# Kernel optimization log

Hardware: AMD Instinct MI355X
Metric: run time of the kernel (lower is better)

## Reference

```python
import jax, jax.numpy as jnp
import numpy as np
from jax import lax

CO, NO, ITERATIONS = 32, 8, 3
STRIDE, PADDING = 1, 1


def squash(x, axis=2):
    # x * ||x|| / (1 + ||x||^2), norm along capsule-dim axis
    norm = jnp.linalg.norm(x, axis=axis, keepdims=True)
    return x * norm / (1.0 + norm * norm)


def setup_inputs() -> dict:
    key = jax.random.key(0)
    k1, k2 = jax.random.split(key)
    x = jax.random.normal(k1, (8, 32, 8, 32, 32), dtype=jnp.float32)
    conv_w = jax.random.normal(k2, (CO * NO, 8, 3, 3), dtype=jnp.float32) * 0.05
    bias = jnp.zeros((CO, NO, 1, 1), dtype=jnp.float32)
    return {"x": x, "conv_w": conv_w, "bias": bias}


def reference(x, conv_w, bias):
    bs, ci, ni, hi, wi = x.shape
    # Conv applied per (batch, input-capsule-channel): [bs*ci, ni, hi, wi]
    xr = x.reshape(bs * ci, ni, hi, wi)
    votes = lax.conv_general_dilated(
        xr, conv_w,
        window_strides=(STRIDE, STRIDE),
        padding=[(PADDING, PADDING), (PADDING, PADDING)],
        dimension_numbers=("NCHW", "OIHW", "NCHW"))
    ho, wo = votes.shape[-2], votes.shape[-1]
    # votes: [bs, ci, co, no, ho, wo]
    votes = votes.reshape(bs, ci, CO, NO, ho, wo)
    logits = jnp.zeros((bs, ci, CO, ho, wo), dtype=votes.dtype)
    activation = None
    for _ in range(ITERATIONS):
        route = jax.nn.softmax(logits, axis=2)  # over co
        # s_j = sum_i c_ij * u_hat_{j|i} + bias -> [bs, co, no, ho, wo]
        preactivate = jnp.sum(route[:, :, :, None] * votes, axis=1) + bias
        activation = squash(preactivate, axis=2)
        # logit update: <u_hat_{j|i}, v_j> summed over no
        distances = jnp.sum(activation[:, None] * votes, axis=3)
        logits = logits + distances
    return activation
```

## Files before the change

### kernel.cpp

```cpp
#include <hip/hip_runtime.h>


typedef __attribute__((ext_vector_type(8))) short short8;
typedef __attribute__((ext_vector_type(4))) float f32x4;

#define LSTR 104
#define KP   96
#define RSTR 36

__device__ __forceinline__ ushort f2bf_rne(float f) {
    unsigned u = __float_as_uint(f);
    return (ushort)((u + 0x7fffu + ((u >> 16) & 1u)) >> 16);
}

__global__ void prep_w(const float* __restrict__ cw, ushort* __restrict__ wp) {
    int e = blockIdx.x * 256 + threadIdx.x;
    int col = e / KP, k = e - col * KP;
    float v = (k < 72) ? cw[col * 72 + k] : 0.0f;
    wp[e] = f2bf_rne(v);
}

__global__ __launch_bounds__(256, 4)
void caps_mfma2(const float* __restrict__ x,
                const ushort* __restrict__ wp,
                const float* __restrict__ bias,
                float* __restrict__ out)
{
    __shared__ ushort A[64 * LSTR];
    __shared__ float  logits[2][32 * 33];
    __shared__ float  routeT[2][32 * RSTR];

    const int t    = threadIdx.x;
    const int braw = blockIdx.x;
    const int bid = ((braw & 7) << 9) | (braw >> 3);
    const int b   = bid >> 9;
    const int q   = bid & 511;
    const int hw0 = q << 1;
    const int h   = hw0 >> 5;
    const int w0  = hw0 & 31;

    {
        const int row = t >> 2, qn = t & 3;
        const int px = row >> 5, ci = row & 31;
        const int wpx = w0 + px;
        const float* xb0 = x + (((size_t)((b * 32 + ci) * 8 + qn * 2)) << 10);
        const float* xb1 = xb0 + 1024;
        ushort hbuf[18];
        #pragma unroll
        for (int kh = 0; kh < 3; ++kh) {
            int hy = h + kh - 1;
            bool vh = (unsigned)hy < 32u;
            int base = hy << 5;
            #pragma unroll
            for (int c = 0; c < 3; ++c) {
                int wx = wpx + c - 1;
                bool ok = vh && ((unsigned)wx < 32u);
                float f0 = ok ? xb0[base + wx] : 0.0f;
                float f1 = ok ? xb1[base + wx] : 0.0f;
                hbuf[kh * 3 + c]     = f2bf_rne(f0);
                hbuf[9 + kh * 3 + c] = f2bf_rne(f1);
            }
        }
        uint* Au = reinterpret_cast<uint*>(A);
        int hbase = row * (LSTR / 2) + qn * 9;
        #pragma unroll
        for (int i = 0; i < 9; ++i)
            Au[hbase + i] = (unsigned)hbuf[2 * i] | ((unsigned)hbuf[2 * i + 1] << 16);
        int pbase = row * (LSTR / 2) + 36 + qn * 4;
        Au[pbase + 0] = 0u; Au[pbase + 1] = 0u;
        Au[pbase + 2] = 0u; Au[pbase + 3] = 0u;
    }
    __syncthreads();

    const int lane = t & 63, wv = t >> 6;
    const int lc = lane & 15, grp = lane >> 4;
    const int no = lane & 7;
    const int par = (lane >> 3) & 1;

    f32x4 acc[4][4];
    #pragma unroll
    for (int mt = 0; mt < 4; ++mt)
        #pragma unroll
        for (int j = 0; j < 4; ++j) acc[mt][j] = (f32x4){0.f, 0.f, 0.f, 0.f};

    #pragma unroll
    for (int ks = 0; ks < 3; ++ks) {
        short8 bq[4];
        #pragma unroll
        for (int j = 0; j < 4; ++j) {
            int col = wv * 64 + j * 16 + lc;
            bq[j] = *reinterpret_cast<const short8*>(wp + col * KP + ks * 32 + grp * 8);
        }
        #pragma unroll
        for (int mt = 0; mt < 4; ++mt) {
            short8 af = *reinterpret_cast<const short8*>(A + (mt * 16 + lc) * LSTR + ks * 32 + grp * 8);
            #pragma unroll
            for (int j = 0; j < 4; ++j)
                acc[mt][j] = __builtin_amdgcn_mfma_f32_16x16x32_bf16(af, bq[j], acc[mt][j], 0, 0, 0);
        }
    }

    float bj[4];
    #pragma unroll
    for (int j = 0; j < 4; ++j) bj[j] = bias[wv * 64 + j * 16 + lc];

    const int ci_s = t >> 3, j_s = t & 7;
    float act_[2][4];

    #pragma unroll
    for (int px = 0; px < 2; ++px) {
        #pragma unroll
        for (int j = 0; j < 4; ++j) {
            const f32x4 a0 = acc[px * 2][j], a1 = acc[px * 2 + 1][j];
            float p = a0[0] + a0[1] + a0[2] + a0[3] + a1[0] + a1[1] + a1[2] + a1[3];
            p += __shfl_xor(p, 16);
            p += __shfl_xor(p, 32);
            p = p * 0.03125f + bj[j];
            float s2 = p * p;
            s2 += __shfl_xor(s2, 1);
            s2 += __shfl_xor(s2, 2);
            s2 += __shfl_xor(s2, 4);
            act_[px][j] = p * sqrtf(s2) / (1.0f + s2);
        }
    }
    #pragma unroll
    for (int px = 0; px < 2; ++px) {
        float* lg = logits[px];
        #pragma unroll
        for (int j = 0; j < 4; ++j) {
            float a = act_[px][j];
            float d[8];
            #pragma unroll
            for (int r = 0; r < 4; ++r) { d[r] = acc[px * 2][j][r] * a; d[4 + r] = acc[px * 2 + 1][j][r] * a; }
            const bool b4 = (no & 4) != 0, b2 = (no & 2) != 0, b1 = (no & 1) != 0;
            float e[4];
            #pragma unroll
            for (int k = 0; k < 4; ++k) {
                float keep = b4 ? d[k + 4] : d[k];
                float send = b4 ? d[k] : d[k + 4];
                e[k] = keep + __shfl_xor(send, 4);
            }
            float f2_[2];
            #pragma unroll
            for (int k = 0; k < 2; ++k) {
                float keep = b2 ? e[k + 2] : e[k];
                float send = b2 ? e[k] : e[k + 2];
                f2_[k] = keep + __shfl_xor(send, 2);
            }
            float keep = b1 ? f2_[1] : f2_[0];
            float send = b1 ? f2_[0] : f2_[1];
            float r = keep + __shfl_xor(send, 1);
            int ci_w = ((no >> 2) << 4) + (grp << 2) + (no & 3);
            int co   = (wv << 3) + 2 * j + par;
            lg[ci_w * 33 + co] = r;
        }
    }
    __syncthreads();

    for (int it = 1; it <= 2; ++it) {
        #pragma unroll
        for (int px = 0; px < 2; ++px) {
            const float* lg = logits[px];
            float* rt = routeT[px];
            float e0 = __expf(lg[ci_s * 33 + j_s]);
            float e1 = __expf(lg[ci_s * 33 + j_s + 8]);
            float e2 = __expf(lg[ci_s * 33 + j_s + 16]);
            float e3 = __expf(lg[ci_s * 33 + j_s + 24]);
            float s = e0 + e1 + e2 + e3;
            s += __shfl_xor(s, 1); s += __shfl_xor(s, 2); s += __shfl_xor(s, 4);
            float inv = 1.0f / s;
            rt[(j_s)      * RSTR + ci_s] = e0 * inv;
            rt[(j_s + 8)  * RSTR + ci_s] = e1 * inv;
            rt[(j_s + 16) * RSTR + ci_s] = e2 * inv;
            rt[(j_s + 24) * RSTR + ci_s] = e3 * inv;
        }
        __syncthreads();

        #pragma unroll
        for (int px = 0; px < 2; ++px) {
            const float* rt = routeT[px];
            #pragma unroll
            for (int j = 0; j < 4; ++j) {
                int co = (wv << 3) + 2 * j + par;
                f32x4 r0 = *reinterpret_cast<const f32x4*>(rt + co * RSTR + grp * 4);
                f32x4 r1 = *reinterpret_cast<const f32x4*>(rt + co * RSTR + 16 + grp * 4);
                float p = 0.0f;
                #pragma unroll
                for (int r = 0; r < 4; ++r) p = fmaf(r0[r], acc[px * 2][j][r], p);
                #pragma unroll
                for (int r = 0; r < 4; ++r) p = fmaf(r1[r], acc[px * 2 + 1][j][r], p);
                p += __shfl_xor(p, 16);
                p += __shfl_xor(p, 32);
                p += bj[j];
                float s2 = p * p;
                s2 += __shfl_xor(s2, 1);
                s2 += __shfl_xor(s2, 2);
                s2 += __shfl_xor(s2, 4);
                act_[px][j] = p * sqrtf(s2) / (1.0f + s2);
            }
        }
        if (it == 2) break;

        #pragma unroll
        for (int px = 0; px < 2; ++px) {
            float* lg = logits[px];
            #pragma unroll
            for (int j = 0; j < 4; ++j) {
                float a = act_[px][j];
                float d[8];
                #pragma unroll
                for (int r = 0; r < 4; ++r) { d[r] = acc[px * 2][j][r] * a; d[4 + r] = acc[px * 2 + 1][j][r] * a; }
                const bool b4 = (no & 4) != 0, b2 = (no & 2) != 0, b1 = (no & 1) != 0;
                float e[4];
                #pragma unroll
                for (int k = 0; k < 4; ++k) {
                    float keep = b4 ? d[k + 4] : d[k];
                    float send = b4 ? d[k] : d[k + 4];
                    e[k] = keep + __shfl_xor(send, 4);
                }
                float f2_[2];
                #pragma unroll
                for (int k = 0; k < 2; ++k) {
                    float keep = b2 ? e[k + 2] : e[k];
                    float send = b2 ? e[k] : e[k + 2];
                    f2_[k] = keep + __shfl_xor(send, 2);
                }
                float keep = b1 ? f2_[1] : f2_[0];
                float send = b1 ? f2_[0] : f2_[1];
                float r = keep + __shfl_xor(send, 1);
                int ci_w = ((no >> 2) << 4) + (grp << 2) + (no & 3);
                int co   = (wv << 3) + 2 * j + par;
                lg[ci_w * 33 + co] += r;
            }
        }
        __syncthreads();
    }

    if (grp == 0) {
        #pragma unroll
        for (int j = 0; j < 4; ++j) {
            int col = wv * 64 + j * 16 + lc;
            float2 v; v.x = act_[0][j]; v.y = act_[1][j];
            *reinterpret_cast<float2*>(out + ((((size_t)b << 8) + col) << 10) + hw0) = v;
        }
    }
}

extern "C" void kernel_launch(void* const* d_in, const int* in_sizes, int n_in,
                              void* d_out, int out_size, void* d_ws, size_t ws_size,
                              hipStream_t stream) {
    const float* x    = (const float*)d_in[0];
    const float* cw   = (const float*)d_in[1];
    const float* bias = (const float*)d_in[2];
    float* out = (float*)d_out;
    ushort* wp = (ushort*)d_ws;
    (void)in_sizes; (void)n_in; (void)out_size; (void)ws_size;
    prep_w<<<96, 256, 0, stream>>>(cw, wp);
    caps_mfma2<<<4096, 256, 0, stream>>>(x, wp, bias, out);
}
```

Measured before the change: 86.72 us.

## Interleave pixel logits in LDS and use fast rcp/sqrt/bf16-pack intrinsics

Result: slower. 147.7 us (+70.3%).

```diff
diff --git a/kernel.cpp b/kernel.cpp
--- a/kernel.cpp
+++ b/kernel.cpp
@@ -7,10 +7,22 @@
 #define LSTR 104
 #define KP   96
 #define RSTR 36
+#define LGS  66
 
 __device__ __forceinline__ ushort f2bf_rne(float f) {
     unsigned u = __float_as_uint(f);
     return (ushort)((u + 0x7fffu + ((u >> 16) & 1u)) >> 16);
+}
+__device__ __forceinline__ float fast_rcp(float x) {
+    float r; asm("v_rcp_f32 %0, %1" : "=v"(r) : "v"(x)); return r;
+}
+__device__ __forceinline__ float fast_sqrt(float x) {
+    float r; asm("v_sqrt_f32 %0, %1" : "=v"(r) : "v"(x)); return r;
+}
+__device__ __forceinline__ unsigned cvt_pk_bf16(float lo, float hi) {
+    unsigned r;
+    asm("v_cvt_pk_bf16_f32 %0, %1, %2" : "=v"(r) : "v"(lo), "v"(hi));
+    return r;
 }
 
 __global__ void prep_w(const float* __restrict__ cw, ushort* __restrict__ wp) {
@@ -27,7 +39,7 @@
                 float* __restrict__ out)
 {
     __shared__ ushort A[64 * LSTR];
-    __shared__ float  logits[2][32 * 33];
+    __shared__ float  lgp[32 * LGS];
     __shared__ float  routeT[2][32 * RSTR];
 
     const int t    = threadIdx.x;
@@ -45,7 +57,7 @@
         const int wpx = w0 + px;
         const float* xb0 = x + (((size_t)((b * 32 + ci) * 8 + qn * 2)) << 10);
         const float* xb1 = xb0 + 1024;
-        ushort hbuf[18];
+        float farr[18];
         #pragma unroll
         for (int kh = 0; kh < 3; ++kh) {
             int hy = h + kh - 1;
@@ -55,17 +67,15 @@
             for (int c = 0; c < 3; ++c) {
                 int wx = wpx + c - 1;
                 bool ok = vh && ((unsigned)wx < 32u);
-                float f0 = ok ? xb0[base + wx] : 0.0f;
-                float f1 = ok ? xb1[base + wx] : 0.0f;
-                hbuf[kh * 3 + c]     = f2bf_rne(f0);
-                hbuf[9 + kh * 3 + c] = f2bf_rne(f1);
+                farr[kh * 3 + c]     = ok ? xb0[base + wx] : 0.0f;
+                farr[9 + kh * 3 + c] = ok ? xb1[base + wx] : 0.0f;
             }
         }
         uint* Au = reinterpret_cast<uint*>(A);
         int hbase = row * (LSTR / 2) + qn * 9;
         #pragma unroll
         for (int i = 0; i < 9; ++i)
-            Au[hbase + i] = (unsigned)hbuf[2 * i] | ((unsigned)hbuf[2 * i + 1] << 16);
+            Au[hbase + i] = cvt_pk_bf16(farr[2 * i], farr[2 * i + 1]);
         int pbase = row * (LSTR / 2) + 36 + qn * 4;
         Au[pbase + 0] = 0u; Au[pbase + 1] = 0u;
         Au[pbase + 2] = 0u; Au[pbase + 3] = 0u;
@@ -105,6 +115,7 @@
     for (int j = 0; j < 4; ++j) bj[j] = bias[wv * 64 + j * 16 + lc];
 
     const int ci_s = t >> 3, j_s = t & 7;
+    const int ci_w = ((no >> 2) << 4) + (grp << 2) + (no & 3);
     float act_[2][4];
 
     #pragma unroll
@@ -120,14 +131,15 @@
             s2 += __shfl_xor(s2, 1);
             s2 += __shfl_xor(s2, 2);
             s2 += __shfl_xor(s2, 4);
-            act_[px][j] = p * sqrtf(s2) / (1.0f + s2);
-        }
-    }
-    #pragma unroll
-    for (int px = 0; px < 2; ++px) {
-        float* lg = logits[px];
-        #pragma unroll
-        for (int j = 0; j < 4; ++j) {
+            act_[px][j] = p * fast_sqrt(s2) * fast_rcp(1.0f + s2);
+        }
+    }
+    #pragma unroll
+    for (int j = 0; j < 4; ++j) {
+        const int co = (wv << 3) + 2 * j + par;
+        float rpx[2];
+        #pragma unroll
+        for (int px = 0; px < 2; ++px) {
             float a = act_[px][j];
             float d[8];
             #pragma unroll
@@ -149,30 +161,42 @@
             }
             float keep = b1 ? f2_[1] : f2_[0];
             float send = b1 ? f2_[0] : f2_[1];
-            float r = keep + __shfl_xor(send, 1);
-            int ci_w = ((no >> 2) << 4) + (grp << 2) + (no & 3);
-            int co   = (wv << 3) + 2 * j + par;
-            lg[ci_w * 33 + co] = r;
-        }
+            rpx[px] = keep + __shfl_xor(send, 1);
+        }
+        float2 v; v.x = rpx[0]; v.y = rpx[1];
+        *(reinterpret_cast<float2*>(lgp + ci_w * LGS) + co) = v;
     }
     __syncthreads();
 
     for (int it = 1; it <= 2; ++it) {
-        #pragma unroll
-        for (int px = 0; px < 2; ++px) {
-            const float* lg = logits[px];
-            float* rt = routeT[px];
-            float e0 = __expf(lg[ci_s * 33 + j_s]);
-            float e1 = __expf(lg[ci_s * 33 + j_s + 8]);
-            float e2 = __expf(lg[ci_s * 33 + j_s + 16]);
-            float e3 = __expf(lg[ci_s * 33 + j_s + 24]);
-            float s = e0 + e1 + e2 + e3;
-            s += __shfl_xor(s, 1); s += __shfl_xor(s, 2); s += __shfl_xor(s, 4);
-            float inv = 1.0f / s;
-            rt[(j_s)      * RSTR + ci_s] = e0 * inv;
-            rt[(j_s + 8)  * RSTR + ci_s] = e1 * inv;
-            rt[(j_s + 16) * RSTR + ci_s] = e2 * inv;
-            rt[(j_s + 24) * RSTR + ci_s] = e3 * inv;
+        {
+            const float2* lrow = reinterpret_cast<const float2*>(lgp + ci_s * LGS);
+            float2 L0 = lrow[j_s], L1 = lrow[j_s + 8];
+            float2 L2 = lrow[j_s + 16], L3 = lrow[j_s + 24];
+            {
+                float e0 = __expf(L0.x), e1 = __expf(L1.x);
+                float e2 = __expf(L2.x), e3 = __expf(L3.x);
+                float s = e0 + e1 + e2 + e3;
+                s += __shfl_xor(s, 1); s += __shfl_xor(s, 2); s += __shfl_xor(s, 4);
+                float inv = fast_rcp(s);
+                float* rt = routeT[0];
+                rt[(j_s)      * RSTR + ci_s] = e0 * inv;
+                rt[(j_s + 8)  * RSTR + ci_s] = e1 * inv;
+                rt[(j_s + 16) * RSTR + ci_s] = e2 * inv;
+                rt[(j_s + 24) * RSTR + ci_s] = e3 * inv;
+            }
+            {
+                float e0 = __expf(L0.y), e1 = __expf(L1.y);
+                float e2 = __expf(L2.y), e3 = __expf(L3.y);
+                float s = e0 + e1 + e2 + e3;
+                s += __shfl_xor(s, 1); s += __shfl_xor(s, 2); s += __shfl_xor(s, 4);
+                float inv = fast_rcp(s);
+                float* rt = routeT[1];
+                rt[(j_s)      * RSTR + ci_s] = e0 * inv;
+                rt[(j_s + 8)  * RSTR + ci_s] = e1 * inv;
+                rt[(j_s + 16) * RSTR + ci_s] = e2 * inv;
+                rt[(j_s + 24) * RSTR + ci_s] = e3 * inv;
+            }
         }
         __syncthreads();
 
@@ -196,16 +220,17 @@
                 s2 += __shfl_xor(s2, 1);
                 s2 += __shfl_xor(s2, 2);
                 s2 += __shfl_xor(s2, 4);
-                act_[px][j] = p * sqrtf(s2) / (1.0f + s2);
+                act_[px][j] = p * fast_sqrt(s2) * fast_rcp(1.0f + s2);
             }
         }
         if (it == 2) break;
 
         #pragma unroll
-        for (int px = 0; px < 2; ++px) {
-            float* lg = logits[px];
-            #pragma unroll
-            for (int j = 0; j < 4; ++j) {
+        for (int j = 0; j < 4; ++j) {
+            const int co = (wv << 3) + 2 * j + par;
+            float rpx[2];
+            #pragma unroll
+            for (int px = 0; px < 2; ++px) {
                 float a = act_[px][j];
                 float d[8];
                 #pragma unroll
@@ -227,11 +252,12 @@
                 }
                 float keep = b1 ? f2_[1] : f2_[0];
                 float send = b1 ? f2_[0] : f2_[1];
-                float r = keep + __shfl_xor(send, 1);
-                int ci_w = ((no >> 2) << 4) + (grp << 2) + (no & 3);
-                int co   = (wv << 3) + 2 * j + par;
-                lg[ci_w * 33 + co] += r;
-            }
+                rpx[px] = keep + __shfl_xor(send, 1);
+            }
+            float2* dst = reinterpret_cast<float2*>(lgp + ci_w * LGS) + co;
+            float2 old = *dst;
+            old.x += rpx[0]; old.y += rpx[1];
+            *dst = old;
         }
         __syncthreads();
     }
```
